# Optimization experiments

Measured on AMD Instinct MI355X. Metric: run time of the kernel, lower is better.

## Reference

```python
import jax, jax.numpy as jnp
import numpy as np

B, N_DEC, M_ENC, D, U = 16, 256, 256, 256, 256

def setup_inputs() -> dict:
    key = jax.random.key(0)
    ks = jax.random.split(key, 6)
    scale = 1.0 / np.sqrt(D)
    return {
        "encoder_output": jax.random.normal(ks[0], (B, M_ENC, D), dtype=jnp.float32),
        "decoder_output": jax.random.normal(ks[1], (B, N_DEC, D), dtype=jnp.float32),
        "W1": jax.random.normal(ks[2], (D, U), dtype=jnp.float32) * scale,
        "b1": jnp.zeros((U,), dtype=jnp.float32),
        "W2": jax.random.normal(ks[3], (D, U), dtype=jnp.float32) * scale,
        "b2": jnp.zeros((U,), dtype=jnp.float32),
        "v_w": jax.random.normal(ks[4], (U, 1), dtype=jnp.float32) * (1.0 / np.sqrt(U)),
        "v_b": jnp.zeros((1,), dtype=jnp.float32),
    }

def reference(encoder_output, decoder_output, W1, b1, W2, b2, v_w, v_b):
    # Project once per sequence, then broadcast (faithful to Dense on expanded dims):
    # enc_proj: [B, M, U], dec_proj: [B, N, U]
    enc_proj = jnp.einsum('bmd,du->bmu', encoder_output, W1) + b1
    dec_proj = jnp.einsum('bnd,du->bnu', decoder_output, W2) + b2
    # score: [B, N, M, U] = tanh(enc_proj[:,None,:,:] + dec_proj[:,:,None,:])
    score = jnp.tanh(enc_proj[:, None, :, :] + dec_proj[:, :, None, :])
    # logits: [B, N, M, 1]; softmax over encoder axis (axis=2)
    logits = jnp.einsum('bnmu,uo->bnmo', score, v_w) + v_b
    attention_weights = jax.nn.softmax(logits, axis=2)
    # context: sum over M of weights * encoder_output -> [B, N, D]
    context_vector = jnp.einsum('bnmo,bmd->bnd', attention_weights, encoder_output)
    return context_vector, attention_weights
```

## Files before the change

### kernel.cpp

```cpp
#include <hip/hip_runtime.h>


constexpr float KSC   = 2.8853900817779268f;
constexpr float LOG2E = 1.4426950408889634f;
constexpr float S16   = 1.52587890625e-05f;
constexpr float LSC   = -3.0517578125e-05f;

struct F4 { float v[4]; };
__device__ __forceinline__ F4 ld4(const float* p) {
    float4 t = *(const float4*)p;
    F4 r; r.v[0] = t.x; r.v[1] = t.y; r.v[2] = t.z; r.v[3] = t.w; return r;
}
__device__ __forceinline__ float rcp_clamp(float v) {
    float r = __builtin_amdgcn_rcpf(v);
    return fminf(fmaxf(r, -1e4f), 1e4f);
}

typedef __attribute__((ext_vector_type(8))) short bf16x8;
typedef __attribute__((ext_vector_type(4))) float f32x4;

__global__ __launch_bounds__(256) void proj_kernel(
    const float* __restrict__ enc, const float* __restrict__ dec,
    const float* __restrict__ W1,  const float* __restrict__ b1,
    const float* __restrict__ W2,  const float* __restrict__ b2,
    const float* __restrict__ vw,
    float* __restrict__ encQ, float* __restrict__ decE)
{
    __shared__ __align__(16) short Ah[64][40], Al[64][40];
    __shared__ __align__(16) short Wh[64][40], Wl[64][40];

    const int tid  = threadIdx.x;
    const int lane = tid & 63;
    const int wv   = tid >> 6;
    const int wr   = wv >> 1, wc = wv & 1;
    const int u0   = blockIdx.x << 6;
    const int rblk = blockIdx.y;
    const bool is_enc = rblk < 64;
    const float* X    = is_enc ? enc : dec;
    const float* Wm   = is_enc ? W1  : W2;
    const float* bias = is_enc ? b1  : b2;
    const int rb = (is_enc ? rblk : rblk - 64) << 6;

    const int r16 = lane & 15;
    const int kg8 = (lane >> 4) << 3;

    f32x4 acc[2][2] = {};

    for (int kt = 0; kt < 256; kt += 32) {
        {
            const int row = tid >> 2, koct = (tid & 3) << 3;
            const float* src = X + (rb + row) * 256 + kt + koct;
            bf16x8 vh, vl;
            #pragma unroll
            for (int j = 0; j < 8; ++j) {
                const float x = src[j];
                const unsigned bx = __float_as_uint(x);
                const float fh = __uint_as_float(bx & 0xFFFF0000u);
                vh[j] = (short)(bx >> 16);
                vl[j] = (short)(__float_as_uint(x - fh) >> 16);
            }
            *reinterpret_cast<bf16x8*>(&Ah[row][koct]) = vh;
            *reinterpret_cast<bf16x8*>(&Al[row][koct]) = vl;
        }
        {
            const int ul = tid & 63, koct = (tid >> 6) << 3;
            const float* src = Wm + (kt + koct) * 256 + u0 + ul;
            bf16x8 vh, vl;
            #pragma unroll
            for (int j = 0; j < 8; ++j) {
                const float x = src[j * 256];
                const unsigned bx = __float_as_uint(x);
                const float fh = __uint_as_float(bx & 0xFFFF0000u);
                vh[j] = (short)(bx >> 16);
                vl[j] = (short)(__float_as_uint(x - fh) >> 16);
            }
            *reinterpret_cast<bf16x8*>(&Wh[ul][koct]) = vh;
            *reinterpret_cast<bf16x8*>(&Wl[ul][koct]) = vl;
        }
        __syncthreads();

        bf16x8 fah[2], fal[2], fbh[2], fbl[2];
        #pragma unroll
        for (int i = 0; i < 2; ++i) {
            const int ar = (wr << 5) + (i << 4) + r16;
            fah[i] = *reinterpret_cast<const bf16x8*>(&Ah[ar][kg8]);
            fal[i] = *reinterpret_cast<const bf16x8*>(&Al[ar][kg8]);
        }
        #pragma unroll
        for (int j = 0; j < 2; ++j) {
            const int wu = (wc << 5) + (j << 4) + r16;
            fbh[j] = *reinterpret_cast<const bf16x8*>(&Wh[wu][kg8]);
            fbl[j] = *reinterpret_cast<const bf16x8*>(&Wl[wu][kg8]);
        }
        #pragma unroll
        for (int i = 0; i < 2; ++i)
            #pragma unroll
            for (int j = 0; j < 2; ++j) {
                acc[i][j] = __builtin_amdgcn_mfma_f32_16x16x32_bf16(
                    fah[i], fbh[j], acc[i][j], 0, 0, 0);
                acc[i][j] = __builtin_amdgcn_mfma_f32_16x16x32_bf16(
                    fah[i], fbl[j], acc[i][j], 0, 0, 0);
                acc[i][j] = __builtin_amdgcn_mfma_f32_16x16x32_bf16(
                    fal[i], fbh[j], acc[i][j], 0, 0, 0);
            }
        __syncthreads();
    }

    const int kg = lane >> 4;
    float bb[2];
    #pragma unroll
    for (int j = 0; j < 2; ++j)
        bb[j] = bias[u0 + (wc << 5) + (j << 4) + r16];

    if (is_enc) {
        #pragma unroll
        for (int i = 0; i < 2; ++i)
            #pragma unroll
            for (int j = 0; j < 2; ++j) {
                const int gu = u0 + (wc << 5) + (j << 4) + r16;
                #pragma unroll
                for (int r = 0; r < 4; ++r) {
                    const int grow = rb + (wr << 5) + (i << 4) + (kg << 2) + r;
                    const int b = grow >> 8, m = grow & 255;
                    const float val = __builtin_amdgcn_exp2f(
                        fmaf(KSC, acc[i][j][r] + bb[j], -16.f));
                    encQ[b * 65536 + (gu >> 2) * 1024 + (m << 2) + (gu & 3)] = val;
                }
            }
    } else {
        float rv[2];
        #pragma unroll
        for (int j = 0; j < 2; ++j)
            rv[j] = rcp_clamp(vw[u0 + (wc << 5) + (j << 4) + r16]);
        #pragma unroll
        for (int i = 0; i < 2; ++i)
            #pragma unroll
            for (int j = 0; j < 2; ++j) {
                const int gu = u0 + (wc << 5) + (j << 4) + r16;
                #pragma unroll
                for (int r = 0; r < 4; ++r) {
                    const int grow = rb + (wr << 5) + (i << 4) + (kg << 2) + r;
                    const float val = __builtin_amdgcn_exp2f(
                        KSC * (acc[i][j][r] + bb[j])) * rv[j];
                    decE[grow * 256 + gu] = val;
                }
            }
    }
}

__global__ __launch_bounds__(512) void logit_kernel(
    const float* __restrict__ encQ,
    const float* __restrict__ decE,
    const float* __restrict__ vw,
    float* __restrict__ logits)
{
    __shared__ float dsD[8][256];
    __shared__ float vcs[256];

    const int tid = threadIdx.x;
    const int b   = blockIdx.y;
    const int n0  = blockIdx.x << 3;
    const int h   = tid >> 8;
    const int m   = tid & 255;
    const int t0  = h << 2;

    {
        const float* dsrc = decE + (b * 256 + n0) * 256;
        #pragma unroll
        for (int i = 0; i < 4; ++i)
            ((float*)dsD)[tid + (i << 9)] = dsrc[tid + (i << 9)];
        if (tid < 256) vcs[tid] = S16 * rcp_clamp(vw[tid]);
    }
    __syncthreads();

    const float* ep = encQ + b * 65536 + (m << 2);
    F4 Ea = ld4(ep);
    F4 Eb = ld4(ep + 1024);
    ep += 2048;

    float acc[4] = {};

    #pragma unroll 4
    for (int o = 0; o < 32; ++o) {
        const F4 Ena = ld4(ep);
        const F4 Enb = ld4(ep + 1024);
        ep += 2048;
        const int u0 = o << 3;
        const F4 ca = ld4(&vcs[u0]);
        const F4 cb = ld4(&vcs[u0 + 4]);
        #pragma unroll
        for (int c = 0; c < 4; ++c) {
            const F4 da = ld4(&dsD[t0 + c][u0]);
            const F4 db = ld4(&dsD[t0 + c][u0 + 4]);
            const float z0 = fmaf(Ea.v[0], da.v[0], ca.v[0]);
            const float z1 = fmaf(Ea.v[1], da.v[1], ca.v[1]);
            const float z2 = fmaf(Ea.v[2], da.v[2], ca.v[2]);
            const float z3 = fmaf(Ea.v[3], da.v[3], ca.v[3]);
            const float y0 = fmaf(Eb.v[0], db.v[0], cb.v[0]);
            const float y1 = fmaf(Eb.v[1], db.v[1], cb.v[1]);
            const float y2 = fmaf(Eb.v[2], db.v[2], cb.v[2]);
            const float y3 = fmaf(Eb.v[3], db.v[3], cb.v[3]);
            const float pz01 = z0 * z1, pz23 = z2 * z3;
            const float py01 = y0 * y1, py23 = y2 * y3;
            const float nz = fmaf(z0 + z1, pz23, (z2 + z3) * pz01);
            const float ny = fmaf(y0 + y1, py23, (y2 + y3) * py01);
            const float pz = pz01 * pz23, py = py01 * py23;
            const float num = fmaf(nz, py, ny * pz);
            acc[c] = fmaf(num, __builtin_amdgcn_rcpf(pz * py), acc[c]);
        }
        Ea = Ena; Eb = Enb;
    }

    #pragma unroll
    for (int c = 0; c < 4; ++c)
        logits[(b * 256 + n0 + t0 + c) * 256 + m] = acc[c] * LSC;
}

__global__ __launch_bounds__(512) void smctx_kernel(
    const float* __restrict__ enc,
    float* __restrict__ out_attn,
    float* __restrict__ out_ctx)
{
    __shared__ float attn_s[8][256];
    __shared__ float redm[8][4], reds[8][4];

    const int tid = threadIdx.x;
    const int b   = blockIdx.y;
    const int n0  = blockIdx.x << 3;
    const int h   = tid >> 8;
    const int m   = tid & 255;
    const int t0  = h << 2;

    float l[4];
    #pragma unroll
    for (int c = 0; c < 4; ++c)
        l[c] = out_attn[(b * 256 + n0 + t0 + c) * 256 + m];

    const int lane = tid & 63, wq = (tid >> 6) & 3;
    #pragma unroll
    for (int c = 0; c < 4; ++c) {
        float x = l[c];
        #pragma unroll
        for (int off = 32; off > 0; off >>= 1)
            x = fmaxf(x, __shfl_xor(x, off));
        if (lane == 0) redm[t0 + c][wq] = x;
    }
    __syncthreads();
    float p[4];
    #pragma unroll
    for (int c = 0; c < 4; ++c) {
        const float mx = fmaxf(fmaxf(redm[t0 + c][0], redm[t0 + c][1]),
                               fmaxf(redm[t0 + c][2], redm[t0 + c][3]));
        p[c] = __builtin_amdgcn_exp2f((l[c] - mx) * LOG2E);
    }
    #pragma unroll
    for (int c = 0; c < 4; ++c) {
        float x = p[c];
        #pragma unroll
        for (int off = 32; off > 0; off >>= 1)
            x += __shfl_xor(x, off);
        if (lane == 0) reds[t0 + c][wq] = x;
    }
    __syncthreads();
    #pragma unroll
    for (int c = 0; c < 4; ++c) {
        const float s = (reds[t0 + c][0] + reds[t0 + c][1])
                      + (reds[t0 + c][2] + reds[t0 + c][3]);
        const float w = p[c] * __builtin_amdgcn_rcpf(s);
        attn_s[t0 + c][m] = w;
        out_attn[(b * 256 + n0 + t0 + c) * 256 + m] = w;
    }
    __syncthreads();

    const float* eb = enc + b * 65536 + m;
    float cx[4] = {};
    #pragma unroll 4
    for (int mm = 0; mm < 256; mm += 4) {
        const float g0 = eb[(mm + 0) << 8];
        const float g1 = eb[(mm + 1) << 8];
        const float g2 = eb[(mm + 2) << 8];
        const float g3 = eb[(mm + 3) << 8];
        #pragma unroll
        for (int c = 0; c < 4; ++c) {
            const F4 aq = ld4(&attn_s[t0 + c][mm]);
            cx[c] = fmaf(aq.v[0], g0, cx[c]);
            cx[c] = fmaf(aq.v[1], g1, cx[c]);
            cx[c] = fmaf(aq.v[2], g2, cx[c]);
            cx[c] = fmaf(aq.v[3], g3, cx[c]);
        }
    }
    #pragma unroll
    for (int c = 0; c < 4; ++c)
        out_ctx[(b * 256 + n0 + t0 + c) * 256 + m] = cx[c];
}

extern "C" void kernel_launch(void* const* d_in, const int* in_sizes, int n_in,
                              void* d_out, int out_size, void* d_ws, size_t ws_size,
                              hipStream_t stream) {
    const float* enc = (const float*)d_in[0];
    const float* dec = (const float*)d_in[1];
    const float* W1  = (const float*)d_in[2];
    const float* b1  = (const float*)d_in[3];
    const float* W2  = (const float*)d_in[4];
    const float* b2  = (const float*)d_in[5];
    const float* vw  = (const float*)d_in[6];

    float* out_ctx  = (float*)d_out;
    float* out_attn = (float*)d_out + 16 * 256 * 256;

    float* encQ = (float*)d_ws;
    float* decE = encQ + 16 * 256 * 256;

    proj_kernel <<<dim3(4, 128), 256, 0, stream>>>(enc, dec, W1, b1, W2, b2, vw, encQ, decE);
    logit_kernel<<<dim3(32, 16), 512, 0, stream>>>(encQ, decE, vw, out_attn);
    smctx_kernel<<<dim3(32, 16), 512, 0, stream>>>(enc, out_attn, out_ctx);
}
```

Before: 132.0 us.

## Pre-split inputs to bf16 hi/lo in a separate kernel and halve logit blocks

A new split_kernel converts the encoder/decoder activations and the weights into bf16 high/low halves once, storing the weights transposed so the projection kernel's tile loads become plain contiguous 16-byte copies instead of strided fp32 loads with per-element splitting. Separately, the logit kernel is split across the encoder axis with a z-dimension of 2 and 256 threads per block, doubling the block count. This trades an extra kernel launch and an extra global round-trip of roughly 8 MB of bf16 data for cheaper projection loads and more parallelism in the logit stage.

```diff
diff --git a/kernel.cpp b/kernel.cpp
--- a/kernel.cpp
+++ b/kernel.cpp
@@ -19,15 +19,43 @@
 typedef __attribute__((ext_vector_type(8))) short bf16x8;
 typedef __attribute__((ext_vector_type(4))) float f32x4;
 
+__global__ __launch_bounds__(256) void split_kernel(
+    const float* __restrict__ enc, const float* __restrict__ dec,
+    const float* __restrict__ W1,  const float* __restrict__ W2,
+    short* __restrict__ Xh, short* __restrict__ Xl,
+    short* __restrict__ WTh, short* __restrict__ WTl)
+{
+    const int idx = blockIdx.x * 256 + threadIdx.x;
+    if (idx < 2097152) {
+        const int row = idx >> 8, k = idx & 255;
+        const float x = (row < 4096) ? enc[row * 256 + k]
+                                     : dec[(row - 4096) * 256 + k];
+        const unsigned bx = __float_as_uint(x);
+        const float fh = __uint_as_float(bx & 0xFFFF0000u);
+        Xh[idx] = (short)(bx >> 16);
+        Xl[idx] = (short)(__float_as_uint(x - fh) >> 16);
+    } else {
+        const int f2 = idx - 2097152;
+        const int t = f2 >> 16, r = f2 & 65535;
+        const int k = r >> 8, u = r & 255;
+        const float x = (t ? W2 : W1)[k * 256 + u];
+        const unsigned bx = __float_as_uint(x);
+        const float fh = __uint_as_float(bx & 0xFFFF0000u);
+        const int o = t * 65536 + u * 256 + k;
+        WTh[o] = (short)(bx >> 16);
+        WTl[o] = (short)(__float_as_uint(x - fh) >> 16);
+    }
+}
+
 __global__ __launch_bounds__(256) void proj_kernel(
-    const float* __restrict__ enc, const float* __restrict__ dec,
-    const float* __restrict__ W1,  const float* __restrict__ b1,
-    const float* __restrict__ W2,  const float* __restrict__ b2,
+    const short* __restrict__ Xh, const short* __restrict__ Xl,
+    const short* __restrict__ WTh, const short* __restrict__ WTl,
+    const float* __restrict__ b1, const float* __restrict__ b2,
     const float* __restrict__ vw,
     float* __restrict__ encQ, float* __restrict__ decE)
 {
     __shared__ __align__(16) short Ah[64][40], Al[64][40];
-    __shared__ __align__(16) short Wh[64][40], Wl[64][40];
+    __shared__ __align__(16) short Bh[64][40], Bl[64][40];
 
     const int tid  = threadIdx.x;
     const int lane = tid & 63;
@@ -36,46 +64,32 @@
     const int u0   = blockIdx.x << 6;
     const int rblk = blockIdx.y;
     const bool is_enc = rblk < 64;
-    const float* X    = is_enc ? enc : dec;
-    const float* Wm   = is_enc ? W1  : W2;
-    const float* bias = is_enc ? b1  : b2;
-    const int rb = (is_enc ? rblk : rblk - 64) << 6;
+    const int rbf = rblk << 6;
+    const int rbt = rbf & 4095;
+    const float* bias = is_enc ? b1 : b2;
+    const int woff = (is_enc ? 0 : 65536);
 
     const int r16 = lane & 15;
     const int kg8 = (lane >> 4) << 3;
 
+    const int srow = tid >> 2, skoct = (tid & 3) << 3;
+
     f32x4 acc[2][2] = {};
 
     for (int kt = 0; kt < 256; kt += 32) {
         {
-            const int row = tid >> 2, koct = (tid & 3) << 3;
-            const float* src = X + (rb + row) * 256 + kt + koct;
-            bf16x8 vh, vl;
-            #pragma unroll
-            for (int j = 0; j < 8; ++j) {
-                const float x = src[j];
-                const unsigned bx = __float_as_uint(x);
-                const float fh = __uint_as_float(bx & 0xFFFF0000u);
-                vh[j] = (short)(bx >> 16);
-                vl[j] = (short)(__float_as_uint(x - fh) >> 16);
-            }
-            *reinterpret_cast<bf16x8*>(&Ah[row][koct]) = vh;
-            *reinterpret_cast<bf16x8*>(&Al[row][koct]) = vl;
+            const int g = (rbf + srow) * 256 + kt + skoct;
+            *reinterpret_cast<bf16x8*>(&Ah[srow][skoct]) =
+                *reinterpret_cast<const bf16x8*>(&Xh[g]);
+            *reinterpret_cast<bf16x8*>(&Al[srow][skoct]) =
+                *reinterpret_cast<const bf16x8*>(&Xl[g]);
         }
         {
-            const int ul = tid & 63, koct = (tid >> 6) << 3;
-            const float* src = Wm + (kt + koct) * 256 + u0 + ul;
-            bf16x8 vh, vl;
-            #pragma unroll
-            for (int j = 0; j < 8; ++j) {
-                const float x = src[j * 256];
-                const unsigned bx = __float_as_uint(x);
-                const float fh = __uint_as_float(bx & 0xFFFF0000u);
-                vh[j] = (short)(bx >> 16);
-                vl[j] = (short)(__float_as_uint(x - fh) >> 16);
-            }
-            *reinterpret_cast<bf16x8*>(&Wh[ul][koct]) = vh;
-            *reinterpret_cast<bf16x8*>(&Wl[ul][koct]) = vl;
+            const int g = woff + (u0 + srow) * 256 + kt + skoct;
+            *reinterpret_cast<bf16x8*>(&Bh[srow][skoct]) =
+                *reinterpret_cast<const bf16x8*>(&WTh[g]);
+            *reinterpret_cast<bf16x8*>(&Bl[srow][skoct]) =
+                *reinterpret_cast<const bf16x8*>(&WTl[g]);
         }
         __syncthreads();
 
@@ -89,8 +103,8 @@
         #pragma unroll
         for (int j = 0; j < 2; ++j) {
             const int wu = (wc << 5) + (j << 4) + r16;
-            fbh[j] = *reinterpret_cast<const bf16x8*>(&Wh[wu][kg8]);
-            fbl[j] = *reinterpret_cast<const bf16x8*>(&Wl[wu][kg8]);
+            fbh[j] = *reinterpret_cast<const bf16x8*>(&Bh[wu][kg8]);
+            fbl[j] = *reinterpret_cast<const bf16x8*>(&Bl[wu][kg8]);
         }
         #pragma unroll
         for (int i = 0; i < 2; ++i)
@@ -120,7 +134,7 @@
                 const int gu = u0 + (wc << 5) + (j << 4) + r16;
                 #pragma unroll
                 for (int r = 0; r < 4; ++r) {
-                    const int grow = rb + (wr << 5) + (i << 4) + (kg << 2) + r;
+                    const int grow = rbt + (wr << 5) + (i << 4) + (kg << 2) + r;
                     const int b = grow >> 8, m = grow & 255;
                     const float val = __builtin_amdgcn_exp2f(
                         fmaf(KSC, acc[i][j][r] + bb[j], -16.f));
@@ -139,7 +153,7 @@
                 const int gu = u0 + (wc << 5) + (j << 4) + r16;
                 #pragma unroll
                 for (int r = 0; r < 4; ++r) {
-                    const int grow = rb + (wr << 5) + (i << 4) + (kg << 2) + r;
+                    const int grow = rbt + (wr << 5) + (i << 4) + (kg << 2) + r;
                     const float val = __builtin_amdgcn_exp2f(
                         KSC * (acc[i][j][r] + bb[j])) * rv[j];
                     decE[grow * 256 + gu] = val;
@@ -148,7 +162,7 @@
     }
 }
 
-__global__ __launch_bounds__(512) void logit_kernel(
+__global__ __launch_bounds__(256) void logit_kernel(
     const float* __restrict__ encQ,
     const float* __restrict__ decE,
     const float* __restrict__ vw,
@@ -160,16 +174,17 @@
     const int tid = threadIdx.x;
     const int b   = blockIdx.y;
     const int n0  = blockIdx.x << 3;
-    const int h   = tid >> 8;
-    const int m   = tid & 255;
+    const int mh  = blockIdx.z;
+    const int h   = tid >> 7;
+    const int m   = (mh << 7) | (tid & 127);
     const int t0  = h << 2;
 
     {
         const float* dsrc = decE + (b * 256 + n0) * 256;
         #pragma unroll
-        for (int i = 0; i < 4; ++i)
-            ((float*)dsD)[tid + (i << 9)] = dsrc[tid + (i << 9)];
-        if (tid < 256) vcs[tid] = S16 * rcp_clamp(vw[tid]);
+        for (int i = 0; i < 8; ++i)
+            ((float*)dsD)[tid + (i << 8)] = dsrc[tid + (i << 8)];
+        vcs[tid] = S16 * rcp_clamp(vw[tid]);
     }
     __syncthreads();
 
@@ -309,9 +324,14 @@
     float* out_attn = (float*)d_out + 16 * 256 * 256;
 
     float* encQ = (float*)d_ws;
-    float* decE = encQ + 16 * 256 * 256;
-
-    proj_kernel <<<dim3(4, 128), 256, 0, stream>>>(enc, dec, W1, b1, W2, b2, vw, encQ, decE);
-    logit_kernel<<<dim3(32, 16), 512, 0, stream>>>(encQ, decE, vw, out_attn);
-    smctx_kernel<<<dim3(32, 16), 512, 0, stream>>>(enc, out_attn, out_ctx);
-}
+    float* decE = encQ + 2097152 / 2;
+    short* Xh   = (short*)(encQ + 2097152);
+    short* Xl   = Xh + 2097152;
+    short* WTh  = Xl + 2097152;
+    short* WTl  = WTh + 131072;
+
+    split_kernel<<<dim3(8704),      256, 0, stream>>>(enc, dec, W1, W2, Xh, Xl, WTh, WTl);
+    proj_kernel <<<dim3(4, 128),    256, 0, stream>>>(Xh, Xl, WTh, WTl, b1, b2, vw, encQ, decE);
+    logit_kernel<<<dim3(32, 16, 2), 256, 0, stream>>>(encQ, decE, vw, out_attn);
+    smctx_kernel<<<dim3(32, 16),    512, 0, stream>>>(enc, out_attn, out_ctx);
+}
```

Measured after the change: 141.8 us. +7.4%, slower.
